# Kernel tuning notes

Hardware: AMD Instinct MI355X
Metric: run time of the kernel (lower is better)

## Reference

```python
import jax, jax.numpy as jnp
import numpy as np

T, B, I, H, LBL = 200, 1024, 128, 128, 4


def setup_inputs() -> dict:
    key = jax.random.key(0)
    ks = jax.random.split(key, 14)
    si = 1.0 / np.sqrt(I)
    sh = 1.0 / np.sqrt(H)
    inputs = jax.random.normal(ks[0], (T, B, I), jnp.float32)
    lengths = jnp.maximum(jax.random.randint(ks[1], (B,), 1, T + 1), LBL).astype(jnp.int32)
    return {
        "inputs": inputs,
        "lengths": lengths,
        "Wih_g": jax.random.normal(ks[2], (3 * H, I), jnp.float32) * si,
        "Whh_g": jax.random.normal(ks[3], (3 * H, H), jnp.float32) * sh,
        "bih_g": jax.random.normal(ks[4], (3 * H,), jnp.float32) * sh,
        "bhh_g": jax.random.normal(ks[5], (3 * H,), jnp.float32) * sh,
        "Wih_l": jax.random.normal(ks[6], (3 * H, I), jnp.float32) * si,
        "Whh_l": jax.random.normal(ks[7], (3 * H, H), jnp.float32) * sh,
        "bih_l": jax.random.normal(ks[8], (3 * H,), jnp.float32) * sh,
        "bhh_l": jax.random.normal(ks[9], (3 * H,), jnp.float32) * sh,
        "A1": jax.random.normal(ks[10], (H, H), jnp.float32) * sh,
        "A2": jax.random.normal(ks[11], (H, H), jnp.float32) * sh,
        "v1": jax.random.normal(ks[12], (1, H), jnp.float32) * sh,
        "label_len": LBL,
    }


def gru(x, Wih, Whh, bih, bhh):
    # x: [T, B, I] time-major. PyTorch GRU cell semantics.
    Bq, Hq = x.shape[1], Whh.shape[1]
    gi_all = jnp.einsum('tbi,gi->tbg', x, Wih) + bih  # precompute input projections [T,B,3H]
    def step(h, gi):
        gh = h @ Whh.T + bhh
        ir, iz, inn = jnp.split(gi, 3, axis=-1)
        hr, hz, hn = jnp.split(gh, 3, axis=-1)
        r = jax.nn.sigmoid(ir + hr)
        z = jax.nn.sigmoid(iz + hz)
        n = jnp.tanh(inn + r * hn)
        h = (1.0 - z) * n + z * h
        return h, h
    h0 = jnp.zeros((Bq, Hq), x.dtype)
    _, hs = jax.lax.scan(step, h0, gi_all)
    return hs  # [T, B, H]


def reference(inputs, lengths, Wih_g, Whh_g, bih_g, bhh_g,
              Wih_l, Whh_l, bih_l, bhh_l, A1, A2, v1, label_len):
    h_g = gru(inputs, Wih_g, Whh_g, bih_g, bhh_g)  # [T,B,H]
    h_l = gru(inputs, Wih_l, Whh_l, bih_l, bhh_l)  # [T,B,H]
    # attention score per step s: v1(sigmoid(A1 h_l + A2 h_g)), query-independent
    pre = jax.nn.sigmoid(jnp.einsum('tbh,gh->tbg', h_l, A1) +
                         jnp.einsum('tbh,gh->tbg', h_g, A2))
    scores = jnp.einsum('tbg,og->tbo', pre, v1)  # [T,B,1]
    # per-t output = cumsum_{s<=t}(score*h_l) + h_g[t]
    out = jnp.cumsum(scores * h_l, axis=0) + h_g  # [T,B,H]
    out_b = jnp.transpose(out, (1, 0, 2))  # [B,T,H]
    # gather last label_len timesteps of each sequence: h[b,k] = out[L_b-label_len+k, b]
    idx = lengths[:, None].astype(jnp.int32) - label_len + jnp.arange(label_len, dtype=jnp.int32)[None, :]
    idx = jnp.clip(idx, 0, out_b.shape[1] - 1)  # [B, label_len]
    h = jnp.take_along_axis(out_b, idx[:, :, None], axis=1)  # [B, label_len, H]
    return h
```

## Files before the change

### kernel.cpp

```cpp
#include <hip/hip_runtime.h>
#include <stdint.h>


typedef __attribute__((ext_vector_type(8))) short short8;
typedef __attribute__((ext_vector_type(4))) float float4v;

#define LDS_BARRIER() asm volatile("s_waitcnt lgkmcnt(0)\n\ts_barrier" ::: "memory")

__device__ inline float bf2f(unsigned short u){
  union { unsigned int i; float f; } v; v.i = ((unsigned int)u) << 16; return v.f;
}
__device__ inline unsigned short f2bf(float f){
  union { float f; unsigned int i; } v; v.f = f;
  unsigned int x = v.i;
  return (unsigned short)((x + 0x7fffu + ((x >> 16) & 1u)) >> 16);
}
__device__ inline unsigned int cvt_pk_bf16(float a, float b){
  unsigned int r;
  asm("v_cvt_pk_bf16_f32 %0, %1, %2" : "=v"(r) : "v"(a), "v"(b));
  return r;
}
__device__ inline float sigm(float x){ return __builtin_amdgcn_rcpf(1.0f + __expf(-x)); }

__global__ void k_prep(unsigned short* hl_slot, unsigned short* hg_slot, float* cum,
                       const float* A1, const float* A2, unsigned short* a12)
{
  int i = blockIdx.x * blockDim.x + threadIdx.x;
  hl_slot[i] = 0;
  hg_slot[i] = 0;
  cum[i] = 0.0f;
  if (i < 32768) {
    a12[i] = f2bf((i < 16384) ? A1[i] : A2[i - 16384]);
  }
}

__global__ __launch_bounds__(512, 2) void k_scan(
    const float* __restrict__ x,
    const float* __restrict__ Wih_g, const float* __restrict__ Whh_g,
    const float* __restrict__ bih_g, const float* __restrict__ bhh_g,
    const float* __restrict__ Wih_l, const float* __restrict__ Whh_l,
    const float* __restrict__ bih_l, const float* __restrict__ bhh_l,
    unsigned short* __restrict__ hl_seq, unsigned short* __restrict__ hg_seq,
    int tc, int t0)
{
  __shared__ __align__(16) unsigned short hbuf[2][16][136];
  __shared__ __align__(16) unsigned short xbuf[2][16][136];
  int tid = threadIdx.x;
  int w = tid >> 6, L = tid & 63, l15 = L & 15, q = L >> 4;
  int gru = blockIdx.x & 1;
  int b0 = (blockIdx.x >> 1) * 16;
  const float* Wih = gru ? Wih_l : Wih_g;
  const float* Whh = gru ? Whh_l : Whh_g;
  const float* bih = gru ? bih_l : bih_g;
  const float* bhh = gru ? bhh_l : bhh_g;
  unsigned short* myseq = gru ? hl_seq : hg_seq;

  int col = w * 16 + l15;

  short8 Wi[3][4], Wh[3][4];
  #pragma unroll
  for (int G = 0; G < 3; G++) {
    int row = G * 128 + col;
    #pragma unroll
    for (int kf = 0; kf < 4; kf++) {
      const float4* p0 = (const float4*)(Wih + (size_t)row * 128 + kf * 32 + q * 8);
      const float4* p1 = (const float4*)(Whh + (size_t)row * 128 + kf * 32 + q * 8);
      float4 a0 = p0[0], a1 = p0[1], b0f = p1[0], b1f = p1[1];
      short8 si, sh;
      si[0]=(short)f2bf(a0.x); si[1]=(short)f2bf(a0.y); si[2]=(short)f2bf(a0.z); si[3]=(short)f2bf(a0.w);
      si[4]=(short)f2bf(a1.x); si[5]=(short)f2bf(a1.y); si[6]=(short)f2bf(a1.z); si[7]=(short)f2bf(a1.w);
      sh[0]=(short)f2bf(b0f.x); sh[1]=(short)f2bf(b0f.y); sh[2]=(short)f2bf(b0f.z); sh[3]=(short)f2bf(b0f.w);
      sh[4]=(short)f2bf(b1f.x); sh[5]=(short)f2bf(b1f.y); sh[6]=(short)f2bf(b1f.z); sh[7]=(short)f2bf(b1f.w);
      Wi[G][kf] = si; Wh[G][kf] = sh;
    }
  }
  float br  = bih[col]       + bhh[col];
  float bz  = bih[128 + col] + bhh[128 + col];
  float bin = bih[256 + col];
  float bnh = bhh[256 + col];

  float hold[4];
  #pragma unroll
  for (int r = 0; r < 4; r++) {
    int m = q * 4 + r;
    unsigned short u = myseq[((size_t)(tc - 1) * 1024 + b0 + m) * 128 + col];
    hold[r] = bf2f(u);
    hbuf[0][m][col] = u;
  }
  int xrow = tid >> 5, xc4 = (tid & 31) * 4;
  {
    float4 x0 = ((const float4*)(x + ((size_t)t0 * 1024 + b0) * 128))[tid];
    *(uint2*)&xbuf[0][xrow][xc4] = make_uint2(cvt_pk_bf16(x0.x, x0.y), cvt_pk_bf16(x0.z, x0.w));
  }
  int tn = t0 + (tc > 1 ? 1 : 0);
  float4 xr = ((const float4*)(x + ((size_t)tn * 1024 + b0) * 128))[tid];
  __syncthreads();

  float4v cx0 = (float4v){0.f,0.f,0.f,0.f}, cx1 = cx0, cx2 = cx0;
  {
    short8 Ax[4];
    #pragma unroll
    for (int kf = 0; kf < 4; kf++) Ax[kf] = *(const short8*)&xbuf[0][l15][kf * 32 + q * 8];
    #pragma unroll
    for (int kf = 0; kf < 4; kf++) cx0 = __builtin_amdgcn_mfma_f32_16x16x32_bf16(Ax[kf], Wi[0][kf], cx0, 0,0,0);
    #pragma unroll
    for (int kf = 0; kf < 4; kf++) cx1 = __builtin_amdgcn_mfma_f32_16x16x32_bf16(Ax[kf], Wi[1][kf], cx1, 0,0,0);
    #pragma unroll
    for (int kf = 0; kf < 4; kf++) cx2 = __builtin_amdgcn_mfma_f32_16x16x32_bf16(Ax[kf], Wi[2][kf], cx2, 0,0,0);
  }
  *(uint2*)&xbuf[1][xrow][xc4] = make_uint2(cvt_pk_bf16(xr.x, xr.y), cvt_pk_bf16(xr.z, xr.w));
  {
    int t2 = t0 + (2 < tc ? 2 : tc - 1);
    xr = ((const float4*)(x + ((size_t)t2 * 1024 + b0) * 128))[tid];
  }
  LDS_BARRIER();

  unsigned short* opq = myseq + ((size_t)(b0 + q * 4)) * 128 + col;

  auto step = [&](int s, int pin, int pout) {
    short8 Ah[4], Axn[4];
    #pragma unroll
    for (int kf = 0; kf < 4; kf++) Ah[kf]  = *(const short8*)&hbuf[pin][l15][kf * 32 + q * 8];
    #pragma unroll
    for (int kf = 0; kf < 4; kf++) Axn[kf] = *(const short8*)&xbuf[pout][l15][kf * 32 + q * 8];

    float4v rh = (float4v){0.f,0.f,0.f,0.f}, zh = rh, nh = rh;
    #pragma unroll
    for (int kf = 0; kf < 4; kf++) rh = __builtin_amdgcn_mfma_f32_16x16x32_bf16(Ah[kf], Wh[0][kf], rh, 0,0,0);
    #pragma unroll
    for (int kf = 0; kf < 4; kf++) zh = __builtin_amdgcn_mfma_f32_16x16x32_bf16(Ah[kf], Wh[1][kf], zh, 0,0,0);
    #pragma unroll
    for (int kf = 0; kf < 4; kf++) nh = __builtin_amdgcn_mfma_f32_16x16x32_bf16(Ah[kf], Wh[2][kf], nh, 0,0,0);

    float4v nx0 = (float4v){0.f,0.f,0.f,0.f}, nx1 = nx0, nx2 = nx0;
    #pragma unroll
    for (int kf = 0; kf < 4; kf++) nx0 = __builtin_amdgcn_mfma_f32_16x16x32_bf16(Axn[kf], Wi[0][kf], nx0, 0,0,0);
    #pragma unroll
    for (int kf = 0; kf < 4; kf++) nx1 = __builtin_amdgcn_mfma_f32_16x16x32_bf16(Axn[kf], Wi[1][kf], nx1, 0,0,0);
    #pragma unroll
    for (int kf = 0; kf < 4; kf++) nx2 = __builtin_amdgcn_mfma_f32_16x16x32_bf16(Axn[kf], Wi[2][kf], nx2, 0,0,0);

    *(uint2*)&xbuf[pin][xrow][xc4] = make_uint2(cvt_pk_bf16(xr.x, xr.y), cvt_pk_bf16(xr.z, xr.w));
    {
      int t3 = t0 + (s + 3 < tc ? s + 3 : tc - 1);
      xr = ((const float4*)(x + ((size_t)t3 * 1024 + b0) * 128))[tid];
    }

    float cr[4], cz[4], cn[4];
    #pragma unroll
    for (int r = 0; r < 4; r++) { cr[r] = cx0[r] + br; cz[r] = cx1[r] + bz; cn[r] = cx2[r] + bin; }

    float hnv[4];
    #pragma unroll
    for (int r = 0; r < 4; r++) {
      float er = __expf(-(rh[r] + cr[r]));
      float ez = __expf(-(zh[r] + cz[r]));
      float pr = 1.0f + er, pz = 1.0f + ez;
      float inv = __builtin_amdgcn_rcpf(pr * pz);
      float rr = pz * inv;
      float zz = pr * inv;
      float y  = cn[r] + rr * (nh[r] + bnh);
      float em = __expf(-2.0f * y);
      float nn = 2.0f * __builtin_amdgcn_rcpf(1.0f + em) - 1.0f;
      hnv[r] = nn + zz * (hold[r] - nn);
      hold[r] = hnv[r];
    }
    unsigned int p01 = cvt_pk_bf16(hnv[0], hnv[1]);
    unsigned int p23 = cvt_pk_bf16(hnv[2], hnv[3]);
    unsigned short h0 = (unsigned short)p01, h1 = (unsigned short)(p01 >> 16);
    unsigned short h2 = (unsigned short)p23, h3 = (unsigned short)(p23 >> 16);
    hbuf[pout][q * 4 + 0][col] = h0;
    hbuf[pout][q * 4 + 1][col] = h1;
    hbuf[pout][q * 4 + 2][col] = h2;
    hbuf[pout][q * 4 + 3][col] = h3;
    opq[0]       = h0;
    opq[128]     = h1;
    opq[256]     = h2;
    opq[384]     = h3;

    cx0 = nx0; cx1 = nx1; cx2 = nx2;
    opq += 131072;
    LDS_BARRIER();
  };

  int s = 0;
  for (; s + 1 < tc; s += 2) { step(s, 0, 1); step(s + 1, 1, 0); }
  if (s < tc) step(s, 0, 1);
}

__global__ __launch_bounds__(512) void k_score(const unsigned short* __restrict__ hl_seq,
                                               const unsigned short* __restrict__ hg_seq,
                                               const unsigned short* __restrict__ a12,
                                               const float* __restrict__ v1,
                                               float* __restrict__ score, int tc)
{
  __shared__ __align__(16) unsigned short M1[128][136];
  __shared__ __align__(16) unsigned short M2[128][136];
  int tid = threadIdx.x;
  int w = tid >> 6, L = tid & 63;
  int l15 = L & 15, q = L >> 4;
  int s = blockIdx.x;
  int bhalf = blockIdx.y * 512;

  #pragma unroll
  for (int it = 0; it < 4; it++) {
    int f8 = it * 512 + tid;
    *(short8*)&M1[f8 >> 4][(f8 & 15) * 8] = *(const short8*)(a12 + (size_t)f8 * 8);
    *(short8*)&M2[f8 >> 4][(f8 & 15) * 8] = *(const short8*)(a12 + 16384 + (size_t)f8 * 8);
  }
  __syncthreads();

  float v1v[8];
  #pragma unroll
  for (int nt = 0; nt < 8; nt++) v1v[nt] = v1[nt * 16 + l15];

  short8 Fl[4], Fg[4], Pl[4], Pg[4];
  {
    size_t base = ((size_t)s * 1024 + bhalf + (size_t)w * 16 + l15) * 128;
    #pragma unroll
    for (int kf = 0; kf < 4; kf++) {
      Fl[kf] = *(const short8*)(hl_seq + base + kf * 32 + q * 8);
      Fg[kf] = *(const short8*)(hg_seq + base + kf * 32 + q * 8);
    }
  }
  #pragma unroll
  for (int it = 0; it < 4; it++) {
    int b0 = bhalf + (it * 8 + w) * 16;
    if (it + 1 < 4) {
      size_t base = ((size_t)s * 1024 + bhalf + (size_t)((it + 1) * 8 + w) * 16 + l15) * 128;
      #pragma unroll
      for (int kf = 0; kf < 4; kf++) {
        Pl[kf] = *(const short8*)(hl_seq + base + kf * 32 + q * 8);
        Pg[kf] = *(const short8*)(hg_seq + base + kf * 32 + q * 8);
      }
    }
    float4v acc[8];
    #pragma unroll
    for (int nt = 0; nt < 8; nt++) {
      float4v a = (float4v){0.f, 0.f, 0.f, 0.f};
      #pragma unroll
      for (int kf = 0; kf < 4; kf++)
        a = __builtin_amdgcn_mfma_f32_16x16x32_bf16(
            Fl[kf], *(const short8*)&M1[nt * 16 + l15][kf * 32 + q * 8], a, 0, 0, 0);
      #pragma unroll
      for (int kf = 0; kf < 4; kf++)
        a = __builtin_amdgcn_mfma_f32_16x16x32_bf16(
            Fg[kf], *(const short8*)&M2[nt * 16 + l15][kf * 32 + q * 8], a, 0, 0, 0);
      acc[nt] = a;
    }
    float p4[4];
    #pragma unroll
    for (int r = 0; r < 4; r++) {
      float sum = 0.f;
      #pragma unroll
      for (int nt = 0; nt < 8; nt++) sum += v1v[nt] * sigm(acc[nt][r]);
      sum += __shfl_xor(sum, 1, 16);
      sum += __shfl_xor(sum, 2, 16);
      sum += __shfl_xor(sum, 4, 16);
      sum += __shfl_xor(sum, 8, 16);
      p4[r] = sum;
    }
    if (l15 == 0) {
      #pragma unroll
      for (int r = 0; r < 4; r++)
        score[(size_t)(b0 + q * 4 + r) * tc + s] = p4[r];
    }
    #pragma unroll
    for (int kf = 0; kf < 4; kf++) { Fl[kf] = Pl[kf]; Fg[kf] = Pg[kf]; }
  }
}

__global__ __launch_bounds__(256) void k_cum(const float* __restrict__ score,
                                             const unsigned short* __restrict__ hl_seq,
                                             const unsigned short* __restrict__ hg_seq,
                                             const int* __restrict__ lengths,
                                             float* __restrict__ cum,
                                             float* __restrict__ out, int tc, int t0)
{
  __shared__ __align__(16) unsigned short hlL[100 * 256];
  __shared__ float scL[2][100];
  int tid = threadIdx.x;
  int b2 = tid >> 7, j = tid & 127;
  int b0 = blockIdx.x * 2;
  int b = b0 + b2;
  int base = b2 * 128 + j;

  float c = cum[(size_t)b * 128 + j];
  int cap0 = lengths[b] - 4;

  float hgv[4];
  #pragma unroll
  for (int d = 0; d < 4; d++) {
    int sl = cap0 + d - t0;
    hgv[d] = (sl >= 0 && sl < tc) ? bf2f(hg_seq[((size_t)sl * 1024 + b) * 128 + j]) : 0.f;
  }

  for (int seg = 0; seg < tc; seg += 100) {
    int len = (tc - seg < 100) ? (tc - seg) : 100;
    __syncthreads();
    for (int f8 = tid; f8 < len * 32; f8 += 256) {
      int sl = f8 >> 5, r8 = f8 & 31;
      *(short8*)&hlL[(size_t)f8 * 8] =
          *(const short8*)(hl_seq + ((size_t)(seg + sl) * 1024 + b0) * 128 + r8 * 8);
    }
    for (int i = tid; i < 2 * len; i += 256) {
      int bb = (i >= len) ? 1 : 0;
      int sl = i - bb * len;
      scL[bb][sl] = score[(size_t)(b0 + bb) * tc + seg + sl];
    }
    __syncthreads();

    int sl = 0;
    for (; sl + 5 <= len; sl += 5) {
      float h[5], sc[5];
      #pragma unroll
      for (int k = 0; k < 5; k++) {
        h[k] = bf2f(hlL[(size_t)(sl + k) * 256 + base]);
        sc[k] = scL[b2][sl + k];
      }
      #pragma unroll
      for (int k = 0; k < 5; k++) {
        c += sc[k] * h[k];
        int d = (t0 + seg + sl + k) - cap0;
        if ((unsigned)d < 4u)
          out[((size_t)b * 4 + d) * 128 + j] = c + hgv[d];
      }
    }
    for (; sl < len; sl++) {
      c += scL[b2][sl] * bf2f(hlL[(size_t)sl * 256 + base]);
      int d = (t0 + seg + sl) - cap0;
      if ((unsigned)d < 4u)
        out[((size_t)b * 4 + d) * 128 + j] = c + hgv[d];
    }
  }
  cum[(size_t)b * 128 + j] = c;
}

extern "C" void kernel_launch(void* const* d_in, const int* in_sizes, int n_in,
                              void* d_out, int out_size, void* d_ws, size_t ws_size,
                              hipStream_t stream)
{
  const float* x     = (const float*)d_in[0];
  const int* lengths = (const int*)d_in[1];
  const float* Wih_g = (const float*)d_in[2];
  const float* Whh_g = (const float*)d_in[3];
  const float* bih_g = (const float*)d_in[4];
  const float* bhh_g = (const float*)d_in[5];
  const float* Wih_l = (const float*)d_in[6];
  const float* Whh_l = (const float*)d_in[7];
  const float* bih_l = (const float*)d_in[8];
  const float* bhh_l = (const float*)d_in[9];
  const float* A1    = (const float*)d_in[10];
  const float* A2    = (const float*)d_in[11];
  const float* v1    = (const float*)d_in[12];
  float* out = (float*)d_out;

  const size_t fixed = 65536 + 524288;
  const int cands[7] = {200, 100, 50, 10, 4, 2, 1};
  int tc = 0;
  for (int i = 0; i < 7; i++) {
    int T = cands[i];
    size_t need = 2 * (size_t)T * 1024 * 128 * 2
                + (size_t)T * 1024 * 4
                + fixed;
    if (need <= ws_size) { tc = T; break; }
  }
  if (!tc) return;

  char* wsb = (char*)d_ws;
  size_t o = 0;
  unsigned short* a12 = (unsigned short*)(wsb + o); o += 65536;
  float* cum   = (float*)(wsb + o); o += 524288;
  unsigned short* hl  = (unsigned short*)(wsb + o); o += (size_t)tc * 1024 * 128 * 2;
  unsigned short* hg  = (unsigned short*)(wsb + o); o += (size_t)tc * 1024 * 128 * 2;
  float* score = (float*)(wsb + o);

  unsigned short* hl_slot = hl + (size_t)(tc - 1) * 1024 * 128;
  unsigned short* hg_slot = hg + (size_t)(tc - 1) * 1024 * 128;

  k_prep<<<512, 256, 0, stream>>>(hl_slot, hg_slot, cum, A1, A2, a12);
  int nch = 200 / tc;
  for (int c = 0; c < nch; c++) {
    k_scan<<<128, 512, 0, stream>>>(x, Wih_g, Whh_g, bih_g, bhh_g,
                                    Wih_l, Whh_l, bih_l, bhh_l, hl, hg, tc, c * tc);
    k_score<<<dim3(tc, 2), 512, 0, stream>>>(hl, hg, a12, v1, score, tc);
    k_cum<<<512, 256, 0, stream>>>(score, hl, hg, lengths, cum, out, tc, c * tc);
  }
}
```

Before: 399.7 us.

## Fuse scan, score and cumsum into one software-pipelined persistent launch

Merges the three per-chunk kernels into one launch whose blocks are split by role: scan blocks for chunk c, score blocks for chunk c-1 and cumsum blocks for chunk c-2, all running concurrently across 6 launches with a fixed chunk size of 50. It also stages the hidden-state global writes through LDS as coalesced 8-byte stores one step late, and keeps the full 200-step history in workspace instead of reusing a ring slot. The goal is to overlap the latency-bound recurrent scan with the score and cumsum work and to cut launch count, at the cost of more workspace, a shared LDS union and fixed problem-size assumptions.

```diff
diff --git a/kernel.cpp b/kernel.cpp
--- a/kernel.cpp
+++ b/kernel.cpp
@@ -22,318 +22,312 @@
 }
 __device__ inline float sigm(float x){ return __builtin_amdgcn_rcpf(1.0f + __expf(-x)); }
 
-__global__ void k_prep(unsigned short* hl_slot, unsigned short* hg_slot, float* cum,
+__global__ void k_prep(unsigned short* zs, float* cum,
                        const float* A1, const float* A2, unsigned short* a12)
 {
   int i = blockIdx.x * blockDim.x + threadIdx.x;
-  hl_slot[i] = 0;
-  hg_slot[i] = 0;
+  zs[i] = 0;
   cum[i] = 0.0f;
   if (i < 32768) {
     a12[i] = f2bf((i < 16384) ? A1[i] : A2[i - 16384]);
   }
 }
 
-__global__ __launch_bounds__(512, 2) void k_scan(
+union __align__(16) LdsU {
+  struct { unsigned short hbuf[2][16][136]; unsigned short xbuf[2][16][136]; } scan;
+  struct { unsigned short M1[128][136]; unsigned short M2[128][136]; } sc;
+  struct { unsigned short hlL[50 * 512]; float scL[4][50]; } cm;
+};
+
+__global__ __launch_bounds__(512, 4) void k_fat(
     const float* __restrict__ x,
     const float* __restrict__ Wih_g, const float* __restrict__ Whh_g,
     const float* __restrict__ bih_g, const float* __restrict__ bhh_g,
     const float* __restrict__ Wih_l, const float* __restrict__ Whh_l,
     const float* __restrict__ bih_l, const float* __restrict__ bhh_l,
-    unsigned short* __restrict__ hl_seq, unsigned short* __restrict__ hg_seq,
-    int tc, int t0)
+    const unsigned short* __restrict__ a12, const float* __restrict__ v1,
+    const int* __restrict__ lengths,
+    unsigned short* __restrict__ hl, unsigned short* __restrict__ hg,
+    const unsigned short* __restrict__ zs,
+    float* __restrict__ score, float* __restrict__ cum, float* __restrict__ out,
+    int scan_t0, int score_t0, int cum_t0)
 {
-  __shared__ __align__(16) unsigned short hbuf[2][16][136];
-  __shared__ __align__(16) unsigned short xbuf[2][16][136];
+  __shared__ LdsU lds;
   int tid = threadIdx.x;
-  int w = tid >> 6, L = tid & 63, l15 = L & 15, q = L >> 4;
-  int gru = blockIdx.x & 1;
-  int b0 = (blockIdx.x >> 1) * 16;
-  const float* Wih = gru ? Wih_l : Wih_g;
-  const float* Whh = gru ? Whh_l : Whh_g;
-  const float* bih = gru ? bih_l : bih_g;
-  const float* bhh = gru ? bhh_l : bhh_g;
-  unsigned short* myseq = gru ? hl_seq : hg_seq;
-
-  int col = w * 16 + l15;
-
-  short8 Wi[3][4], Wh[3][4];
-  #pragma unroll
-  for (int G = 0; G < 3; G++) {
-    int row = G * 128 + col;
-    #pragma unroll
-    for (int kf = 0; kf < 4; kf++) {
-      const float4* p0 = (const float4*)(Wih + (size_t)row * 128 + kf * 32 + q * 8);
-      const float4* p1 = (const float4*)(Whh + (size_t)row * 128 + kf * 32 + q * 8);
-      float4 a0 = p0[0], a1 = p0[1], b0f = p1[0], b1f = p1[1];
-      short8 si, sh;
-      si[0]=(short)f2bf(a0.x); si[1]=(short)f2bf(a0.y); si[2]=(short)f2bf(a0.z); si[3]=(short)f2bf(a0.w);
-      si[4]=(short)f2bf(a1.x); si[5]=(short)f2bf(a1.y); si[6]=(short)f2bf(a1.z); si[7]=(short)f2bf(a1.w);
-      sh[0]=(short)f2bf(b0f.x); sh[1]=(short)f2bf(b0f.y); sh[2]=(short)f2bf(b0f.z); sh[3]=(short)f2bf(b0f.w);
-      sh[4]=(short)f2bf(b1f.x); sh[5]=(short)f2bf(b1f.y); sh[6]=(short)f2bf(b1f.z); sh[7]=(short)f2bf(b1f.w);
-      Wi[G][kf] = si; Wh[G][kf] = sh;
-    }
-  }
-  float br  = bih[col]       + bhh[col];
-  float bz  = bih[128 + col] + bhh[128 + col];
-  float bin = bih[256 + col];
-  float bnh = bhh[256 + col];
-
-  float hold[4];
-  #pragma unroll
-  for (int r = 0; r < 4; r++) {
-    int m = q * 4 + r;
-    unsigned short u = myseq[((size_t)(tc - 1) * 1024 + b0 + m) * 128 + col];
-    hold[r] = bf2f(u);
-    hbuf[0][m][col] = u;
-  }
-  int xrow = tid >> 5, xc4 = (tid & 31) * 4;
+  int bid = blockIdx.x;
+
+  if (bid < 128) {
+    if (scan_t0 < 0) return;
+    const int tc = 50;
+    int t0 = scan_t0;
+    auto& hbuf = lds.scan.hbuf;
+    auto& xbuf = lds.scan.xbuf;
+
+    int w = tid >> 6, L = tid & 63, l15 = L & 15, q = L >> 4;
+    int gru = bid & 1;
+    int b0 = (bid >> 1) * 16;
+    const float* Wih = gru ? Wih_l : Wih_g;
+    const float* Whh = gru ? Whh_l : Whh_g;
+    const float* bih = gru ? bih_l : bih_g;
+    const float* bhh = gru ? bhh_l : bhh_g;
+    unsigned short* myseq = gru ? hl : hg;
+
+    int col = w * 16 + l15;
+
+    short8 Wi[3][4], Wh[3][4];
+    #pragma unroll
+    for (int G = 0; G < 3; G++) {
+      int row = G * 128 + col;
+      #pragma unroll
+      for (int kf = 0; kf < 4; kf++) {
+        const float4* p0 = (const float4*)(Wih + (size_t)row * 128 + kf * 32 + q * 8);
+        const float4* p1 = (const float4*)(Whh + (size_t)row * 128 + kf * 32 + q * 8);
+        float4 a0 = p0[0], a1 = p0[1], b0f = p1[0], b1f = p1[1];
+        short8 si, sh;
+        si[0]=(short)f2bf(a0.x); si[1]=(short)f2bf(a0.y); si[2]=(short)f2bf(a0.z); si[3]=(short)f2bf(a0.w);
+        si[4]=(short)f2bf(a1.x); si[5]=(short)f2bf(a1.y); si[6]=(short)f2bf(a1.z); si[7]=(short)f2bf(a1.w);
+        sh[0]=(short)f2bf(b0f.x); sh[1]=(short)f2bf(b0f.y); sh[2]=(short)f2bf(b0f.z); sh[3]=(short)f2bf(b0f.w);
+        sh[4]=(short)f2bf(b1f.x); sh[5]=(short)f2bf(b1f.y); sh[6]=(short)f2bf(b1f.z); sh[7]=(short)f2bf(b1f.w);
+        Wi[G][kf] = si; Wh[G][kf] = sh;
+      }
+    }
+    float br  = bih[col]       + bhh[col];
+    float bz  = bih[128 + col] + bhh[128 + col];
+    float bin = bih[256 + col];
+    float bnh = bhh[256 + col];
+
+    const unsigned short* carry = (t0 == 0) ? zs : (myseq + (size_t)(t0 - 1) * 131072);
+    float hold[4];
+    #pragma unroll
+    for (int r = 0; r < 4; r++) {
+      int m = q * 4 + r;
+      unsigned short u = carry[(size_t)(b0 + m) * 128 + col];
+      hold[r] = bf2f(u);
+      hbuf[0][m][col] = u;
+    }
+    int xrow = tid >> 5, xc4 = (tid & 31) * 4;
+    size_t hoff = (size_t)b0 * 128 + xrow * 128 + xc4;
+    {
+      float4 x0 = ((const float4*)(x + ((size_t)t0 * 1024 + b0) * 128))[tid];
+      *(uint2*)&xbuf[0][xrow][xc4] = make_uint2(cvt_pk_bf16(x0.x, x0.y), cvt_pk_bf16(x0.z, x0.w));
+    }
+    float4 xr = ((const float4*)(x + ((size_t)(t0 + 1) * 1024 + b0) * 128))[tid];
+    __syncthreads();
+
+    float4v cx0 = (float4v){0.f,0.f,0.f,0.f}, cx1 = cx0, cx2 = cx0;
+    {
+      short8 Ax[4];
+      #pragma unroll
+      for (int kf = 0; kf < 4; kf++) Ax[kf] = *(const short8*)&xbuf[0][l15][kf * 32 + q * 8];
+      #pragma unroll
+      for (int kf = 0; kf < 4; kf++) cx0 = __builtin_amdgcn_mfma_f32_16x16x32_bf16(Ax[kf], Wi[0][kf], cx0, 0,0,0);
+      #pragma unroll
+      for (int kf = 0; kf < 4; kf++) cx1 = __builtin_amdgcn_mfma_f32_16x16x32_bf16(Ax[kf], Wi[1][kf], cx1, 0,0,0);
+      #pragma unroll
+      for (int kf = 0; kf < 4; kf++) cx2 = __builtin_amdgcn_mfma_f32_16x16x32_bf16(Ax[kf], Wi[2][kf], cx2, 0,0,0);
+    }
+    *(uint2*)&xbuf[1][xrow][xc4] = make_uint2(cvt_pk_bf16(xr.x, xr.y), cvt_pk_bf16(xr.z, xr.w));
+    xr = ((const float4*)(x + ((size_t)(t0 + 2) * 1024 + b0) * 128))[tid];
+    LDS_BARRIER();
+
+    auto step = [&](int s, int pin, int pout) {
+      short8 Ah[4], Axn[4];
+      #pragma unroll
+      for (int kf = 0; kf < 4; kf++) Ah[kf]  = *(const short8*)&hbuf[pin][l15][kf * 32 + q * 8];
+      #pragma unroll
+      for (int kf = 0; kf < 4; kf++) Axn[kf] = *(const short8*)&xbuf[pout][l15][kf * 32 + q * 8];
+
+      if (s > 0) {
+        uint2 hv = *(const uint2*)&hbuf[pin][xrow][xc4];
+        *(uint2*)(myseq + (size_t)(t0 + s - 1) * 131072 + hoff) = hv;
+      }
+
+      float4v rh = (float4v){0.f,0.f,0.f,0.f}, zh = rh, nh = rh;
+      #pragma unroll
+      for (int kf = 0; kf < 4; kf++) rh = __builtin_amdgcn_mfma_f32_16x16x32_bf16(Ah[kf], Wh[0][kf], rh, 0,0,0);
+      #pragma unroll
+      for (int kf = 0; kf < 4; kf++) zh = __builtin_amdgcn_mfma_f32_16x16x32_bf16(Ah[kf], Wh[1][kf], zh, 0,0,0);
+      #pragma unroll
+      for (int kf = 0; kf < 4; kf++) nh = __builtin_amdgcn_mfma_f32_16x16x32_bf16(Ah[kf], Wh[2][kf], nh, 0,0,0);
+
+      float4v nx0 = (float4v){0.f,0.f,0.f,0.f}, nx1 = nx0, nx2 = nx0;
+      #pragma unroll
+      for (int kf = 0; kf < 4; kf++) nx0 = __builtin_amdgcn_mfma_f32_16x16x32_bf16(Axn[kf], Wi[0][kf], nx0, 0,0,0);
+      #pragma unroll
+      for (int kf = 0; kf < 4; kf++) nx1 = __builtin_amdgcn_mfma_f32_16x16x32_bf16(Axn[kf], Wi[1][kf], nx1, 0,0,0);
+      #pragma unroll
+      for (int kf = 0; kf < 4; kf++) nx2 = __builtin_amdgcn_mfma_f32_16x16x32_bf16(Axn[kf], Wi[2][kf], nx2, 0,0,0);
+
+      *(uint2*)&xbuf[pin][xrow][xc4] = make_uint2(cvt_pk_bf16(xr.x, xr.y), cvt_pk_bf16(xr.z, xr.w));
+      {
+        int t3 = t0 + (s + 3 < tc ? s + 3 : tc - 1);
+        xr = ((const float4*)(x + ((size_t)t3 * 1024 + b0) * 128))[tid];
+      }
+
+      float cr[4], cz[4], cn[4];
+      #pragma unroll
+      for (int r = 0; r < 4; r++) { cr[r] = cx0[r] + br; cz[r] = cx1[r] + bz; cn[r] = cx2[r] + bin; }
+
+      float hnv[4];
+      #pragma unroll
+      for (int r = 0; r < 4; r++) {
+        float er = __expf(-(rh[r] + cr[r]));
+        float ez = __expf(-(zh[r] + cz[r]));
+        float pr = 1.0f + er, pz = 1.0f + ez;
+        float inv = __builtin_amdgcn_rcpf(pr * pz);
+        float rr = pz * inv;
+        float zz = pr * inv;
+        float y  = cn[r] + rr * (nh[r] + bnh);
+        float em = __expf(-2.0f * y);
+        float nn = 2.0f * __builtin_amdgcn_rcpf(1.0f + em) - 1.0f;
+        hnv[r] = nn + zz * (hold[r] - nn);
+        hold[r] = hnv[r];
+      }
+      unsigned int p01 = cvt_pk_bf16(hnv[0], hnv[1]);
+      unsigned int p23 = cvt_pk_bf16(hnv[2], hnv[3]);
+      hbuf[pout][q * 4 + 0][col] = (unsigned short)p01;
+      hbuf[pout][q * 4 + 1][col] = (unsigned short)(p01 >> 16);
+      hbuf[pout][q * 4 + 2][col] = (unsigned short)p23;
+      hbuf[pout][q * 4 + 3][col] = (unsigned short)(p23 >> 16);
+
+      cx0 = nx0; cx1 = nx1; cx2 = nx2;
+      LDS_BARRIER();
+    };
+
+    for (int s = 0; s + 1 < tc; s += 2) { step(s, 0, 1); step(s + 1, 1, 0); }
+    {
+      uint2 hv = *(const uint2*)&hbuf[tc & 1][xrow][xc4];
+      *(uint2*)(myseq + (size_t)(t0 + tc - 1) * 131072 + hoff) = hv;
+    }
+    return;
+  }
+
+  if (bid < 228) {
+    if (score_t0 < 0) return;
+    int rb = bid - 128;
+    int w = tid >> 6, L = tid & 63;
+    int l15 = L & 15, q = L >> 4;
+    int s = score_t0 + (rb >> 1);
+    int bhalf = (rb & 1) * 512;
+    auto& M1 = lds.sc.M1;
+    auto& M2 = lds.sc.M2;
+
+    #pragma unroll
+    for (int it = 0; it < 4; it++) {
+      int f8 = it * 512 + tid;
+      *(short8*)&M1[f8 >> 4][(f8 & 15) * 8] = *(const short8*)(a12 + (size_t)f8 * 8);
+      *(short8*)&M2[f8 >> 4][(f8 & 15) * 8] = *(const short8*)(a12 + 16384 + (size_t)f8 * 8);
+    }
+    __syncthreads();
+
+    float v1v[8];
+    #pragma unroll
+    for (int nt = 0; nt < 8; nt++) v1v[nt] = v1[nt * 16 + l15];
+
+    short8 Fl[4], Fg[4], Pl[4], Pg[4];
+    {
+      size_t base = ((size_t)s * 1024 + bhalf + (size_t)w * 16 + l15) * 128;
+      #pragma unroll
+      for (int kf = 0; kf < 4; kf++) {
+        Fl[kf] = *(const short8*)(hl + base + kf * 32 + q * 8);
+        Fg[kf] = *(const short8*)(hg + base + kf * 32 + q * 8);
+      }
+    }
+    #pragma unroll
+    for (int it = 0; it < 4; it++) {
+      int b0s = bhalf + (it * 8 + w) * 16;
+      if (it + 1 < 4) {
+        size_t base = ((size_t)s * 1024 + bhalf + (size_t)((it + 1) * 8 + w) * 16 + l15) * 128;
+        #pragma unroll
+        for (int kf = 0; kf < 4; kf++) {
+          Pl[kf] = *(const short8*)(hl + base + kf * 32 + q * 8);
+          Pg[kf] = *(const short8*)(hg + base + kf * 32 + q * 8);
+        }
+      }
+      float4v acc[8];
+      #pragma unroll
+      for (int nt = 0; nt < 8; nt++) {
+        float4v a = (float4v){0.f, 0.f, 0.f, 0.f};
+        #pragma unroll
+        for (int kf = 0; kf < 4; kf++)
+          a = __builtin_amdgcn_mfma_f32_16x16x32_bf16(
+              Fl[kf], *(const short8*)&M1[nt * 16 + l15][kf * 32 + q * 8], a, 0, 0, 0);
+        #pragma unroll
+        for (int kf = 0; kf < 4; kf++)
+          a = __builtin_amdgcn_mfma_f32_16x16x32_bf16(
+              Fg[kf], *(const short8*)&M2[nt * 16 + l15][kf * 32 + q * 8], a, 0, 0, 0);
+        acc[nt] = a;
+      }
+      float p4[4];
+      #pragma unroll
+      for (int r = 0; r < 4; r++) {
+        float sum = 0.f;
+        #pragma unroll
+        for (int nt = 0; nt < 8; nt++) sum += v1v[nt] * sigm(acc[nt][r]);
+        sum += __shfl_xor(sum, 1, 16);
+        sum += __shfl_xor(sum, 2, 16);
+        sum += __shfl_xor(sum, 4, 16);
+        sum += __shfl_xor(sum, 8, 16);
+        p4[r] = sum;
+      }
+      if (l15 == 0) {
+        #pragma unroll
+        for (int r = 0; r < 4; r++)
+          score[(size_t)(b0s + q * 4 + r) * 200 + s] = p4[r];
+      }
+      #pragma unroll
+      for (int kf = 0; kf < 4; kf++) { Fl[kf] = Pl[kf]; Fg[kf] = Pg[kf]; }
+    }
+    return;
+  }
+
+  if (cum_t0 < 0) return;
   {
-    float4 x0 = ((const float4*)(x + ((size_t)t0 * 1024 + b0) * 128))[tid];
-    *(uint2*)&xbuf[0][xrow][xc4] = make_uint2(cvt_pk_bf16(x0.x, x0.y), cvt_pk_bf16(x0.z, x0.w));
-  }
-  int tn = t0 + (tc > 1 ? 1 : 0);
-  float4 xr = ((const float4*)(x + ((size_t)tn * 1024 + b0) * 128))[tid];
-  __syncthreads();
-
-  float4v cx0 = (float4v){0.f,0.f,0.f,0.f}, cx1 = cx0, cx2 = cx0;
-  {
-    short8 Ax[4];
-    #pragma unroll
-    for (int kf = 0; kf < 4; kf++) Ax[kf] = *(const short8*)&xbuf[0][l15][kf * 32 + q * 8];
-    #pragma unroll
-    for (int kf = 0; kf < 4; kf++) cx0 = __builtin_amdgcn_mfma_f32_16x16x32_bf16(Ax[kf], Wi[0][kf], cx0, 0,0,0);
-    #pragma unroll
-    for (int kf = 0; kf < 4; kf++) cx1 = __builtin_amdgcn_mfma_f32_16x16x32_bf16(Ax[kf], Wi[1][kf], cx1, 0,0,0);
-    #pragma unroll
-    for (int kf = 0; kf < 4; kf++) cx2 = __builtin_amdgcn_mfma_f32_16x16x32_bf16(Ax[kf], Wi[2][kf], cx2, 0,0,0);
-  }
-  *(uint2*)&xbuf[1][xrow][xc4] = make_uint2(cvt_pk_bf16(xr.x, xr.y), cvt_pk_bf16(xr.z, xr.w));
-  {
-    int t2 = t0 + (2 < tc ? 2 : tc - 1);
-    xr = ((const float4*)(x + ((size_t)t2 * 1024 + b0) * 128))[tid];
-  }
-  LDS_BARRIER();
-
-  unsigned short* opq = myseq + ((size_t)(b0 + q * 4)) * 128 + col;
-
-  auto step = [&](int s, int pin, int pout) {
-    short8 Ah[4], Axn[4];
-    #pragma unroll
-    for (int kf = 0; kf < 4; kf++) Ah[kf]  = *(const short8*)&hbuf[pin][l15][kf * 32 + q * 8];
-    #pragma unroll
-    for (int kf = 0; kf < 4; kf++) Axn[kf] = *(const short8*)&xbuf[pout][l15][kf * 32 + q * 8];
-
-    float4v rh = (float4v){0.f,0.f,0.f,0.f}, zh = rh, nh = rh;
-    #pragma unroll
-    for (int kf = 0; kf < 4; kf++) rh = __builtin_amdgcn_mfma_f32_16x16x32_bf16(Ah[kf], Wh[0][kf], rh, 0,0,0);
-    #pragma unroll
-    for (int kf = 0; kf < 4; kf++) zh = __builtin_amdgcn_mfma_f32_16x16x32_bf16(Ah[kf], Wh[1][kf], zh, 0,0,0);
-    #pragma unroll
-    for (int kf = 0; kf < 4; kf++) nh = __builtin_amdgcn_mfma_f32_16x16x32_bf16(Ah[kf], Wh[2][kf], nh, 0,0,0);
-
-    float4v nx0 = (float4v){0.f,0.f,0.f,0.f}, nx1 = nx0, nx2 = nx0;
-    #pragma unroll
-    for (int kf = 0; kf < 4; kf++) nx0 = __builtin_amdgcn_mfma_f32_16x16x32_bf16(Axn[kf], Wi[0][kf], nx0, 0,0,0);
-    #pragma unroll
-    for (int kf = 0; kf < 4; kf++) nx1 = __builtin_amdgcn_mfma_f32_16x16x32_bf16(Axn[kf], Wi[1][kf], nx1, 0,0,0);
-    #pragma unroll
-    for (int kf = 0; kf < 4; kf++) nx2 = __builtin_amdgcn_mfma_f32_16x16x32_bf16(Axn[kf], Wi[2][kf], nx2, 0,0,0);
-
-    *(uint2*)&xbuf[pin][xrow][xc4] = make_uint2(cvt_pk_bf16(xr.x, xr.y), cvt_pk_bf16(xr.z, xr.w));
-    {
-      int t3 = t0 + (s + 3 < tc ? s + 3 : tc - 1);
-      xr = ((const float4*)(x + ((size_t)t3 * 1024 + b0) * 128))[tid];
-    }
-
-    float cr[4], cz[4], cn[4];
-    #pragma unroll
-    for (int r = 0; r < 4; r++) { cr[r] = cx0[r] + br; cz[r] = cx1[r] + bz; cn[r] = cx2[r] + bin; }
-
-    float hnv[4];
-    #pragma unroll
-    for (int r = 0; r < 4; r++) {
-      float er = __expf(-(rh[r] + cr[r]));
-      float ez = __expf(-(zh[r] + cz[r]));
-      float pr = 1.0f + er, pz = 1.0f + ez;
-      float inv = __builtin_amdgcn_rcpf(pr * pz);
-      float rr = pz * inv;
-      float zz = pr * inv;
-      float y  = cn[r] + rr * (nh[r] + bnh);
-      float em = __expf(-2.0f * y);
-      float nn = 2.0f * __builtin_amdgcn_rcpf(1.0f + em) - 1.0f;
-      hnv[r] = nn + zz * (hold[r] - nn);
-      hold[r] = hnv[r];
-    }
-    unsigned int p01 = cvt_pk_bf16(hnv[0], hnv[1]);
-    unsigned int p23 = cvt_pk_bf16(hnv[2], hnv[3]);
-    unsigned short h0 = (unsigned short)p01, h1 = (unsigned short)(p01 >> 16);
-    unsigned short h2 = (unsigned short)p23, h3 = (unsigned short)(p23 >> 16);
-    hbuf[pout][q * 4 + 0][col] = h0;
-    hbuf[pout][q * 4 + 1][col] = h1;
-    hbuf[pout][q * 4 + 2][col] = h2;
-    hbuf[pout][q * 4 + 3][col] = h3;
-    opq[0]       = h0;
-    opq[128]     = h1;
-    opq[256]     = h2;
-    opq[384]     = h3;
-
-    cx0 = nx0; cx1 = nx1; cx2 = nx2;
-    opq += 131072;
-    LDS_BARRIER();
-  };
-
-  int s = 0;
-  for (; s + 1 < tc; s += 2) { step(s, 0, 1); step(s + 1, 1, 0); }
-  if (s < tc) step(s, 0, 1);
-}
-
-__global__ __launch_bounds__(512) void k_score(const unsigned short* __restrict__ hl_seq,
-                                               const unsigned short* __restrict__ hg_seq,
-                                               const unsigned short* __restrict__ a12,
-                                               const float* __restrict__ v1,
-                                               float* __restrict__ score, int tc)
-{
-  __shared__ __align__(16) unsigned short M1[128][136];
-  __shared__ __align__(16) unsigned short M2[128][136];
-  int tid = threadIdx.x;
-  int w = tid >> 6, L = tid & 63;
-  int l15 = L & 15, q = L >> 4;
-  int s = blockIdx.x;
-  int bhalf = blockIdx.y * 512;
-
-  #pragma unroll
-  for (int it = 0; it < 4; it++) {
-    int f8 = it * 512 + tid;
-    *(short8*)&M1[f8 >> 4][(f8 & 15) * 8] = *(const short8*)(a12 + (size_t)f8 * 8);
-    *(short8*)&M2[f8 >> 4][(f8 & 15) * 8] = *(const short8*)(a12 + 16384 + (size_t)f8 * 8);
-  }
-  __syncthreads();
-
-  float v1v[8];
-  #pragma unroll
-  for (int nt = 0; nt < 8; nt++) v1v[nt] = v1[nt * 16 + l15];
-
-  short8 Fl[4], Fg[4], Pl[4], Pg[4];
-  {
-    size_t base = ((size_t)s * 1024 + bhalf + (size_t)w * 16 + l15) * 128;
-    #pragma unroll
-    for (int kf = 0; kf < 4; kf++) {
-      Fl[kf] = *(const short8*)(hl_seq + base + kf * 32 + q * 8);
-      Fg[kf] = *(const short8*)(hg_seq + base + kf * 32 + q * 8);
-    }
-  }
-  #pragma unroll
-  for (int it = 0; it < 4; it++) {
-    int b0 = bhalf + (it * 8 + w) * 16;
-    if (it + 1 < 4) {
-      size_t base = ((size_t)s * 1024 + bhalf + (size_t)((it + 1) * 8 + w) * 16 + l15) * 128;
-      #pragma unroll
-      for (int kf = 0; kf < 4; kf++) {
-        Pl[kf] = *(const short8*)(hl_seq + base + kf * 32 + q * 8);
-        Pg[kf] = *(const short8*)(hg_seq + base + kf * 32 + q * 8);
-      }
-    }
-    float4v acc[8];
-    #pragma unroll
-    for (int nt = 0; nt < 8; nt++) {
-      float4v a = (float4v){0.f, 0.f, 0.f, 0.f};
-      #pragma unroll
-      for (int kf = 0; kf < 4; kf++)
-        a = __builtin_amdgcn_mfma_f32_16x16x32_bf16(
-            Fl[kf], *(const short8*)&M1[nt * 16 + l15][kf * 32 + q * 8], a, 0, 0, 0);
-      #pragma unroll
-      for (int kf = 0; kf < 4; kf++)
-        a = __builtin_amdgcn_mfma_f32_16x16x32_bf16(
-            Fg[kf], *(const short8*)&M2[nt * 16 + l15][kf * 32 + q * 8], a, 0, 0, 0);
-      acc[nt] = a;
-    }
-    float p4[4];
-    #pragma unroll
-    for (int r = 0; r < 4; r++) {
-      float sum = 0.f;
-      #pragma unroll
-      for (int nt = 0; nt < 8; nt++) sum += v1v[nt] * sigm(acc[nt][r]);
-      sum += __shfl_xor(sum, 1, 16);
-      sum += __shfl_xor(sum, 2, 16);
-      sum += __shfl_xor(sum, 4, 16);
-      sum += __shfl_xor(sum, 8, 16);
-      p4[r] = sum;
-    }
-    if (l15 == 0) {
-      #pragma unroll
-      for (int r = 0; r < 4; r++)
-        score[(size_t)(b0 + q * 4 + r) * tc + s] = p4[r];
-    }
-    #pragma unroll
-    for (int kf = 0; kf < 4; kf++) { Fl[kf] = Pl[kf]; Fg[kf] = Pg[kf]; }
-  }
-}
-
-__global__ __launch_bounds__(256) void k_cum(const float* __restrict__ score,
-                                             const unsigned short* __restrict__ hl_seq,
-                                             const unsigned short* __restrict__ hg_seq,
-                                             const int* __restrict__ lengths,
-                                             float* __restrict__ cum,
-                                             float* __restrict__ out, int tc, int t0)
-{
-  __shared__ __align__(16) unsigned short hlL[100 * 256];
-  __shared__ float scL[2][100];
-  int tid = threadIdx.x;
-  int b2 = tid >> 7, j = tid & 127;
-  int b0 = blockIdx.x * 2;
-  int b = b0 + b2;
-  int base = b2 * 128 + j;
-
-  float c = cum[(size_t)b * 128 + j];
-  int cap0 = lengths[b] - 4;
-
-  float hgv[4];
-  #pragma unroll
-  for (int d = 0; d < 4; d++) {
-    int sl = cap0 + d - t0;
-    hgv[d] = (sl >= 0 && sl < tc) ? bf2f(hg_seq[((size_t)sl * 1024 + b) * 128 + j]) : 0.f;
-  }
-
-  for (int seg = 0; seg < tc; seg += 100) {
-    int len = (tc - seg < 100) ? (tc - seg) : 100;
+    int rb = bid - 228;
+    int b4 = tid >> 7, j = tid & 127;
+    int b0c = rb * 4;
+    int b = b0c + b4;
+    int t0c = cum_t0;
+
+    float c = cum[(size_t)b * 128 + j];
+    int cap0 = lengths[b] - 4;
+
+    float hgv[4];
+    #pragma unroll
+    for (int d = 0; d < 4; d++) {
+      int sl = cap0 + d - t0c;
+      hgv[d] = (sl >= 0 && sl < 50) ? bf2f(hg[((size_t)(cap0 + d) * 1024 + b) * 128 + j]) : 0.f;
+    }
+
+    for (int f8 = tid; f8 < 50 * 64; f8 += 512) {
+      int sl = f8 >> 6, r8 = f8 & 63;
+      *(short8*)&lds.cm.hlL[(size_t)f8 * 8] =
+          *(const short8*)(hl + ((size_t)(t0c + sl) * 1024 + b0c) * 128 + r8 * 8);
+    }
+    for (int i = tid; i < 4 * 50; i += 512) {
+      int bb = i / 50, sl = i - bb * 50;
+      lds.cm.scL[bb][sl] = score[(size_t)(b0c + bb) * 200 + t0c + sl];
+    }
     __syncthreads();
-    for (int f8 = tid; f8 < len * 32; f8 += 256) {
-      int sl = f8 >> 5, r8 = f8 & 31;
-      *(short8*)&hlL[(size_t)f8 * 8] =
-          *(const short8*)(hl_seq + ((size_t)(seg + sl) * 1024 + b0) * 128 + r8 * 8);
-    }
-    for (int i = tid; i < 2 * len; i += 256) {
-      int bb = (i >= len) ? 1 : 0;
-      int sl = i - bb * len;
-      scL[bb][sl] = score[(size_t)(b0 + bb) * tc + seg + sl];
-    }
-    __syncthreads();
-
-    int sl = 0;
-    for (; sl + 5 <= len; sl += 5) {
-      float h[5], sc[5];
+
+    int base = b4 * 128 + j;
+    for (int sl = 0; sl < 50; sl += 5) {
+      float h[5], scv[5];
       #pragma unroll
       for (int k = 0; k < 5; k++) {
-        h[k] = bf2f(hlL[(size_t)(sl + k) * 256 + base]);
-        sc[k] = scL[b2][sl + k];
+        h[k] = bf2f(lds.cm.hlL[(size_t)(sl + k) * 512 + base]);
+        scv[k] = lds.cm.scL[b4][sl + k];
       }
       #pragma unroll
       for (int k = 0; k < 5; k++) {
-        c += sc[k] * h[k];
-        int d = (t0 + seg + sl + k) - cap0;
+        c += scv[k] * h[k];
+        int d = (t0c + sl + k) - cap0;
         if ((unsigned)d < 4u)
           out[((size_t)b * 4 + d) * 128 + j] = c + hgv[d];
       }
     }
-    for (; sl < len; sl++) {
-      c += scL[b2][sl] * bf2f(hlL[(size_t)sl * 256 + base]);
-      int d = (t0 + seg + sl) - cap0;
-      if ((unsigned)d < 4u)
-        out[((size_t)b * 4 + d) * 128 + j] = c + hgv[d];
-    }
-  }
-  cum[(size_t)b * 128 + j] = c;
+    cum[(size_t)b * 128 + j] = c;
+  }
 }
 
 extern "C" void kernel_launch(void* const* d_in, const int* in_sizes, int n_in,
@@ -355,35 +349,26 @@
   const float* v1    = (const float*)d_in[12];
   float* out = (float*)d_out;
 
-  const size_t fixed = 65536 + 524288;
-  const int cands[7] = {200, 100, 50, 10, 4, 2, 1};
-  int tc = 0;
-  for (int i = 0; i < 7; i++) {
-    int T = cands[i];
-    size_t need = 2 * (size_t)T * 1024 * 128 * 2
-                + (size_t)T * 1024 * 4
-                + fixed;
-    if (need <= ws_size) { tc = T; break; }
-  }
-  if (!tc) return;
-
+  const int TC = 50;
   char* wsb = (char*)d_ws;
   size_t o = 0;
   unsigned short* a12 = (unsigned short*)(wsb + o); o += 65536;
-  float* cum   = (float*)(wsb + o); o += 524288;
-  unsigned short* hl  = (unsigned short*)(wsb + o); o += (size_t)tc * 1024 * 128 * 2;
-  unsigned short* hg  = (unsigned short*)(wsb + o); o += (size_t)tc * 1024 * 128 * 2;
-  float* score = (float*)(wsb + o);
-
-  unsigned short* hl_slot = hl + (size_t)(tc - 1) * 1024 * 128;
-  unsigned short* hg_slot = hg + (size_t)(tc - 1) * 1024 * 128;
-
-  k_prep<<<512, 256, 0, stream>>>(hl_slot, hg_slot, cum, A1, A2, a12);
-  int nch = 200 / tc;
-  for (int c = 0; c < nch; c++) {
-    k_scan<<<128, 512, 0, stream>>>(x, Wih_g, Whh_g, bih_g, bhh_g,
-                                    Wih_l, Whh_l, bih_l, bhh_l, hl, hg, tc, c * tc);
-    k_score<<<dim3(tc, 2), 512, 0, stream>>>(hl, hg, a12, v1, score, tc);
-    k_cum<<<512, 256, 0, stream>>>(score, hl, hg, lengths, cum, out, tc, c * tc);
-  }
-}
+  float* cum          = (float*)(wsb + o);          o += 524288;
+  unsigned short* zs  = (unsigned short*)(wsb + o); o += 262144;
+  unsigned short* hl  = (unsigned short*)(wsb + o); o += (size_t)200 * 1024 * 128 * 2;
+  unsigned short* hg  = (unsigned short*)(wsb + o); o += (size_t)200 * 1024 * 128 * 2;
+  float* score        = (float*)(wsb + o);          o += (size_t)1024 * 200 * 4;
+  if (o > ws_size) return;
+
+  k_prep<<<512, 256, 0, stream>>>(zs, cum, A1, A2, a12);
+
+  for (int Lh = 0; Lh < 6; Lh++) {
+    int st0 = (Lh < 4) ? Lh * TC : -1;
+    int sc0 = (Lh >= 1 && Lh <= 4) ? (Lh - 1) * TC : -1;
+    int cu0 = (Lh >= 2) ? (Lh - 2) * TC : -1;
+    k_fat<<<484, 512, 0, stream>>>(x, Wih_g, Whh_g, bih_g, bhh_g,
+                                   Wih_l, Whh_l, bih_l, bhh_l,
+                                   a12, v1, lengths, hl, hg, zs,
+                                   score, cum, out, st0, sc0, cu0);
+  }
+}
```

Measured after the change: 1.042 ms. +160.7%, slower.
